# Optimization experiments

Measured on AMD Instinct MI355X. Metric: run time of the kernel, lower is better.

## Reference

```python
import jax, jax.numpy as jnp
import numpy as np

B, S, D = 524288, 10, 6  # batch of independent tiny attention problems; original module is one [10,6] sample


def setup_inputs() -> dict:
    key = jax.random.key(0)
    ks = jax.random.split(key, 7)
    bound = 1.0 / np.sqrt(D)  # torch nn.Linear default init range
    x = jax.random.normal(ks[0], (B, S, D), dtype=jnp.float32)
    Wk = jax.random.uniform(ks[1], (D, D), jnp.float32, -bound, bound)
    bk = jax.random.uniform(ks[2], (D,), jnp.float32, -bound, bound)
    Wq = jax.random.uniform(ks[3], (D, D), jnp.float32, -bound, bound)
    bq = jax.random.uniform(ks[4], (D,), jnp.float32, -bound, bound)
    Wv = jax.random.uniform(ks[5], (D, D), jnp.float32, -bound, bound)
    bv = jax.random.uniform(ks[6], (D,), jnp.float32, -bound, bound)
    return {"x": x, "Wk": Wk, "bk": bk, "Wq": Wq, "bq": bq, "Wv": Wv, "bv": bv}


def reference(x, Wk, bk, Wq, bq, Wv, bv):
    # Linear layers (torch stores W as [out,in]; y = x W^T + b)
    k = jnp.einsum('bsd,ed->bse', x, Wk) + bk  # [B,S,D]
    q = jnp.einsum('bsd,ed->bse', x, Wq) + bq
    v = jnp.einsum('bsd,ed->bse', x, Wv) + bv
    # per-query attention over the 10 keys (no scaling in original)
    scores = jax.nn.softmax(jnp.einsum('bqd,bkd->bqk', q, k), axis=-1)  # [B,S,S]
    out = jnp.einsum('bqk,bkd->bqd', scores, v)  # [B,S,D]
    # original sums attended vector over feature dim -> one scalar per query
    return jnp.sum(out, axis=-1)  # [B,S]
```

## Files before the change

kernel.cpp:

```cpp
#include <hip/hip_runtime.h>


#define NB 524288
#define S 10
#define D 6

__global__ void precompute_kernel(const float* __restrict__ Wk, const float* __restrict__ bk,
                                  const float* __restrict__ Wq, const float* __restrict__ bq,
                                  const float* __restrict__ Wv, const float* __restrict__ bv,
                                  float* __restrict__ ws) {
    int t = threadIdx.x;
    if (t < 36) {
        int d = t / 6, dp = t % 6;
        float g = 0.f;
        for (int e = 0; e < D; ++e) g += Wq[e * D + d] * Wk[e * D + dp];
        ws[t] = g;
    } else if (t < 42) {
        int dp = t - 36;
        float s = 0.f;
        for (int e = 0; e < D; ++e) s += bq[e] * Wk[e * D + dp];
        ws[t] = s;
    } else if (t < 48) {
        int d = t - 42;
        float s = 0.f;
        for (int e = 0; e < D; ++e) s += Wv[e * D + d];
        ws[t] = s;
    } else if (t == 48) {
        float s = 0.f;
        for (int e = 0; e < D; ++e) s += bv[e];
        ws[t] = s;
    }
}

__global__ __launch_bounds__(256) void attn_kernel(const float* __restrict__ x,
                                                   const float* __restrict__ ws,
                                                   float* __restrict__ out) {
    int b = blockIdx.x * blockDim.x + threadIdx.x;
    if (b >= NB) return;

    float G[36], w[6], wvs[6];
    #pragma unroll
    for (int i = 0; i < 36; ++i) G[i] = ws[i];
    #pragma unroll
    for (int i = 0; i < 6; ++i) w[i] = ws[36 + i];
    #pragma unroll
    for (int i = 0; i < 6; ++i) wvs[i] = ws[42 + i];
    float bvs = ws[48];

    const float4* xp = (const float4*)(x + (size_t)b * (S * D));
    float xv[S * D];
    #pragma unroll
    for (int i = 0; i < 15; ++i) {
        float4 v = xp[i];
        xv[4 * i + 0] = v.x;
        xv[4 * i + 1] = v.y;
        xv[4 * i + 2] = v.z;
        xv[4 * i + 3] = v.w;
    }

    float z[S * D], a[S], vs[S];
    #pragma unroll
    for (int k = 0; k < S; ++k) {
        #pragma unroll
        for (int d = 0; d < D; ++d) {
            float zz = 0.f;
            #pragma unroll
            for (int dp = 0; dp < D; ++dp) zz += G[d * 6 + dp] * xv[k * D + dp];
            z[k * D + d] = zz;
        }
        float ak = 0.f, vk = bvs;
        #pragma unroll
        for (int dp = 0; dp < D; ++dp) {
            ak += w[dp] * xv[k * D + dp];
            vk += wvs[dp] * xv[k * D + dp];
        }
        a[k] = ak;
        vs[k] = vk;
    }

    float o[S];
    #pragma unroll
    for (int q = 0; q < S; ++q) {
        float num = 0.f, den = 0.f;
        #pragma unroll
        for (int k = 0; k < S; ++k) {
            float s = a[k];
            #pragma unroll
            for (int d = 0; d < D; ++d) s += xv[q * D + d] * z[k * D + d];
            float e = __expf(s);
            den += e;
            num += e * vs[k];
        }
        o[q] = num * __builtin_amdgcn_rcpf(den);
    }

    float2* op = (float2*)(out + (size_t)b * S);
    #pragma unroll
    for (int i = 0; i < 5; ++i) op[i] = make_float2(o[2 * i + 0], o[2 * i + 1]);
}

extern "C" void kernel_launch(void* const* d_in, const int* in_sizes, int n_in,
                              void* d_out, int out_size, void* d_ws, size_t ws_size,
                              hipStream_t stream) {
    const float* x  = (const float*)d_in[0];
    const float* Wk = (const float*)d_in[1];
    const float* bk = (const float*)d_in[2];
    const float* Wq = (const float*)d_in[3];
    const float* bq = (const float*)d_in[4];
    const float* Wv = (const float*)d_in[5];
    const float* bv = (const float*)d_in[6];
    float* out = (float*)d_out;
    float* ws  = (float*)d_ws;

    precompute_kernel<<<1, 64, 0, stream>>>(Wk, bk, Wq, bq, Wv, bv, ws);
    attn_kernel<<<NB / 256, 256, 0, stream>>>(x, ws, out);
}
```

Measured before the change: 42.52 us.

## Stage inputs through padded LDS and split each batch item across two threads

Each block now loads 128 batch items with coalesced float4 reads into LDS rows padded to 61 floats, then assigns two threads per item, each handling five queries. Query-side projection (x_q·G) replaces the per-key z computation, so each thread holds far fewer registers. The goal is coalesced global loads, fewer VGPRs and higher occupancy (launch bounds request 5 waves), in exchange for redundant key-side work across the thread pair, LDS traffic and a block barrier. Output writes become stride-5 scalar stores.

```diff
diff --git a/kernel.cpp b/kernel.cpp
--- a/kernel.cpp
+++ b/kernel.cpp
@@ -4,6 +4,9 @@
 #define NB 524288
 #define S 10
 #define D 6
+#define TPB 256
+#define EPB 128
+#define ROW 61
 
 __global__ void precompute_kernel(const float* __restrict__ Wk, const float* __restrict__ bk,
                                   const float* __restrict__ Wq, const float* __restrict__ bq,
@@ -32,11 +35,12 @@
     }
 }
 
-__global__ __launch_bounds__(256) void attn_kernel(const float* __restrict__ x,
-                                                   const float* __restrict__ ws,
-                                                   float* __restrict__ out) {
-    int b = blockIdx.x * blockDim.x + threadIdx.x;
-    if (b >= NB) return;
+__global__ __launch_bounds__(TPB, 5) void attn_kernel(const float* __restrict__ x,
+                                                      const float* __restrict__ ws,
+                                                      float* __restrict__ out) {
+    __shared__ float xs[EPB * ROW];
+    const int t = threadIdx.x;
+    const int blk = blockIdx.x;
 
     float G[36], w[6], wvs[6];
     #pragma unroll
@@ -45,58 +49,65 @@
     for (int i = 0; i < 6; ++i) w[i] = ws[36 + i];
     #pragma unroll
     for (int i = 0; i < 6; ++i) wvs[i] = ws[42 + i];
-    float bvs = ws[48];
+    const float bvs = ws[48];
 
-    const float4* xp = (const float4*)(x + (size_t)b * (S * D));
-    float xv[S * D];
+    const float4* xg = (const float4*)x + (size_t)blk * (EPB * 15);
     #pragma unroll
-    for (int i = 0; i < 15; ++i) {
-        float4 v = xp[i];
-        xv[4 * i + 0] = v.x;
-        xv[4 * i + 1] = v.y;
-        xv[4 * i + 2] = v.z;
-        xv[4 * i + 3] = v.w;
+    for (int i = 0; i < 8; ++i) {
+        int f = t + TPB * i;
+        if (f < EPB * 15) {
+            float4 v = xg[f];
+            int e = f / 15, sub = f - e * 15;
+            float* dst = &xs[e * ROW + sub * 4];
+            dst[0] = v.x; dst[1] = v.y; dst[2] = v.z; dst[3] = v.w;
+        }
+    }
+    __syncthreads();
+
+    const int e = t >> 1;
+    const int h = t & 1;
+    const float* xe = &xs[e * ROW];
+
+    float tq[5][6];
+    #pragma unroll
+    for (int j = 0; j < 5; ++j) {
+        int q = h * 5 + j;
+        float xq[6];
+        #pragma unroll
+        for (int d = 0; d < 6; ++d) xq[d] = xe[q * 6 + d];
+        #pragma unroll
+        for (int dp = 0; dp < 6; ++dp) {
+            float s = 0.f;
+            #pragma unroll
+            for (int d = 0; d < 6; ++d) s += xq[d] * G[d * 6 + dp];
+            tq[j][dp] = s;
+        }
     }
 
-    float z[S * D], a[S], vs[S];
+    float num[5] = {0.f, 0.f, 0.f, 0.f, 0.f};
+    float den[5] = {0.f, 0.f, 0.f, 0.f, 0.f};
     #pragma unroll
     for (int k = 0; k < S; ++k) {
+        float xk[6];
         #pragma unroll
-        for (int d = 0; d < D; ++d) {
-            float zz = 0.f;
+        for (int d = 0; d < 6; ++d) xk[d] = xe[k * 6 + d];
+        float a = 0.f, vk = bvs;
+        #pragma unroll
+        for (int d = 0; d < 6; ++d) { a += w[d] * xk[d]; vk += wvs[d] * xk[d]; }
+        #pragma unroll
+        for (int j = 0; j < 5; ++j) {
+            float s = a;
             #pragma unroll
-            for (int dp = 0; dp < D; ++dp) zz += G[d * 6 + dp] * xv[k * D + dp];
-            z[k * D + d] = zz;
+            for (int d = 0; d < 6; ++d) s += tq[j][d] * xk[d];
+            float ex = __expf(s);
+            den[j] += ex;
+            num[j] += ex * vk;
         }
-        float ak = 0.f, vk = bvs;
-        #pragma unroll
-        for (int dp = 0; dp < D; ++dp) {
-            ak += w[dp] * xv[k * D + dp];
-            vk += wvs[dp] * xv[k * D + dp];
-        }
-        a[k] = ak;
-        vs[k] = vk;
     }
 
-    float o[S];
+    float* op = out + (size_t)blk * (EPB * S) + t * 5;
     #pragma unroll
-    for (int q = 0; q < S; ++q) {
-        float num = 0.f, den = 0.f;
-        #pragma unroll
-        for (int k = 0; k < S; ++k) {
-            float s = a[k];
-            #pragma unroll
-            for (int d = 0; d < D; ++d) s += xv[q * D + d] * z[k * D + d];
-            float e = __expf(s);
-            den += e;
-            num += e * vs[k];
-        }
-        o[q] = num * __builtin_amdgcn_rcpf(den);
-    }
-
-    float2* op = (float2*)(out + (size_t)b * S);
-    #pragma unroll
-    for (int i = 0; i < 5; ++i) op[i] = make_float2(o[2 * i + 0], o[2 * i + 1]);
+    for (int j = 0; j < 5; ++j) op[j] = num[j] * __builtin_amdgcn_rcpf(den[j]);
 }
 
 extern "C" void kernel_launch(void* const* d_in, const int* in_sizes, int n_in,
@@ -113,5 +124,5 @@
     float* ws  = (float*)d_ws;
 
     precompute_kernel<<<1, 64, 0, stream>>>(Wk, bk, Wq, bq, Wv, bv, ws);
-    attn_kernel<<<NB / 256, 256, 0, stream>>>(x, ws, out);
+    attn_kernel<<<NB / EPB, TPB, 0, stream>>>(x, ws, out);
 }
```

After: 127.7 us. 200% more time.

## Process four elements per thread with double-buffered register prefetch

Applied to the files above, without the earlier changes.

Each thread now handles four batch elements spaced a grid apart, loading the next element's 60 floats into a second register buffer while computing the current one. Weights are read through readfirstlane so they stay in scalar registers, and log2(e) is folded into the precomputed Gram matrix so exp2 replaces expf. The aim is to hide global load latency and cut per-thread setup, at the cost of higher register pressure (two 60-float buffers) and a quarter as many threads. The launch bound now requests two blocks per CU.

```diff
diff --git a/kernel.cpp b/kernel.cpp
--- a/kernel.cpp
+++ b/kernel.cpp
@@ -4,22 +4,29 @@
 #define NB 524288
 #define S 10
 #define D 6
+#define XFL 60
+#define TPB 256
+#define EPT 4
+#define NTHREADS (NB / EPT)
+#define NBLK (NTHREADS / TPB)
+#define ESTRIDE NTHREADS
 
 __global__ void precompute_kernel(const float* __restrict__ Wk, const float* __restrict__ bk,
                                   const float* __restrict__ Wq, const float* __restrict__ bq,
                                   const float* __restrict__ Wv, const float* __restrict__ bv,
                                   float* __restrict__ ws) {
+    const float LOG2E = 1.44269504088896340736f;
     int t = threadIdx.x;
     if (t < 36) {
         int d = t / 6, dp = t % 6;
         float g = 0.f;
         for (int e = 0; e < D; ++e) g += Wq[e * D + d] * Wk[e * D + dp];
-        ws[t] = g;
+        ws[t] = g * LOG2E;
     } else if (t < 42) {
         int dp = t - 36;
         float s = 0.f;
         for (int e = 0; e < D; ++e) s += bq[e] * Wk[e * D + dp];
-        ws[t] = s;
+        ws[t] = s * LOG2E;
     } else if (t < 48) {
         int d = t - 42;
         float s = 0.f;
@@ -32,71 +39,90 @@
     }
 }
 
-__global__ __launch_bounds__(256) void attn_kernel(const float* __restrict__ x,
-                                                   const float* __restrict__ ws,
-                                                   float* __restrict__ out) {
-    int b = blockIdx.x * blockDim.x + threadIdx.x;
-    if (b >= NB) return;
+__device__ __forceinline__ float sconst(const float* __restrict__ p, int i) {
+    return __int_as_float(__builtin_amdgcn_readfirstlane(__float_as_int(p[i])));
+}
+
+#define LOAD_ELEM(buf, eidx)                                                 \
+    {                                                                        \
+        const float4* _p = (const float4*)(x + (size_t)(eidx) * XFL);        \
+        _Pragma("unroll")                                                    \
+        for (int _i = 0; _i < 15; ++_i) {                                    \
+            float4 _v = _p[_i];                                              \
+            buf[4 * _i + 0] = _v.x;                                          \
+            buf[4 * _i + 1] = _v.y;                                          \
+            buf[4 * _i + 2] = _v.z;                                          \
+            buf[4 * _i + 3] = _v.w;                                          \
+        }                                                                    \
+    }
+
+#define COMPUTE_ELEM(xv, eidx)                                               \
+    {                                                                        \
+        float z[XFL], a[S], vs[S];                                           \
+        _Pragma("unroll")                                                    \
+        for (int _k = 0; _k < S; ++_k) {                                     \
+            float _ak = 0.f, _vk = bvs;                                      \
+            _Pragma("unroll")                                                \
+            for (int _d = 0; _d < D; ++_d) {                                 \
+                float _xk = xv[_k * D + _d];                                 \
+                _ak += w[_d] * _xk;                                          \
+                _vk += wvs[_d] * _xk;                                        \
+            }                                                                \
+            a[_k] = _ak; vs[_k] = _vk;                                       \
+            _Pragma("unroll")                                                \
+            for (int _d = 0; _d < D; ++_d) {                                 \
+                float _zz = 0.f;                                             \
+                _Pragma("unroll")                                            \
+                for (int _dp = 0; _dp < D; ++_dp)                            \
+                    _zz += G[_d * D + _dp] * xv[_k * D + _dp];               \
+                z[_k * D + _d] = _zz;                                        \
+            }                                                                \
+        }                                                                    \
+        float o[S];                                                          \
+        _Pragma("unroll")                                                    \
+        for (int _q = 0; _q < S; ++_q) {                                     \
+            float _num = 0.f, _den = 0.f;                                    \
+            _Pragma("unroll")                                                \
+            for (int _k = 0; _k < S; ++_k) {                                 \
+                float _s = a[_k];                                            \
+                _Pragma("unroll")                                            \
+                for (int _d = 0; _d < D; ++_d)                               \
+                    _s += xv[_q * D + _d] * z[_k * D + _d];                  \
+                float _ex = __builtin_amdgcn_exp2f(_s);                      \
+                _den += _ex; _num += _ex * vs[_k];                           \
+            }                                                                \
+            o[_q] = _num * __builtin_amdgcn_rcpf(_den);                      \
+        }                                                                    \
+        float2* _op = (float2*)(out + (size_t)(eidx) * S);                   \
+        _Pragma("unroll")                                                    \
+        for (int _i = 0; _i < 5; ++_i)                                       \
+            _op[_i] = make_float2(o[2 * _i], o[2 * _i + 1]);                 \
+    }
+
+__global__ __launch_bounds__(TPB, 2) void attn_kernel(const float* __restrict__ x,
+                                                      const float* __restrict__ ws,
+                                                      float* __restrict__ out) {
+    const int g = blockIdx.x * TPB + threadIdx.x;
 
     float G[36], w[6], wvs[6];
     #pragma unroll
-    for (int i = 0; i < 36; ++i) G[i] = ws[i];
+    for (int i = 0; i < 36; ++i) G[i] = sconst(ws, i);
     #pragma unroll
-    for (int i = 0; i < 6; ++i) w[i] = ws[36 + i];
+    for (int i = 0; i < 6; ++i) w[i] = sconst(ws, 36 + i);
     #pragma unroll
-    for (int i = 0; i < 6; ++i) wvs[i] = ws[42 + i];
-    float bvs = ws[48];
+    for (int i = 0; i < 6; ++i) wvs[i] = sconst(ws, 42 + i);
+    const float bvs = sconst(ws, 48);
 
-    const float4* xp = (const float4*)(x + (size_t)b * (S * D));
-    float xv[S * D];
-    #pragma unroll
-    for (int i = 0; i < 15; ++i) {
-        float4 v = xp[i];
-        xv[4 * i + 0] = v.x;
-        xv[4 * i + 1] = v.y;
-        xv[4 * i + 2] = v.z;
-        xv[4 * i + 3] = v.w;
-    }
+    float bufA[XFL], bufB[XFL];
 
-    float z[S * D], a[S], vs[S];
-    #pragma unroll
-    for (int k = 0; k < S; ++k) {
-        #pragma unroll
-        for (int d = 0; d < D; ++d) {
-            float zz = 0.f;
-            #pragma unroll
-            for (int dp = 0; dp < D; ++dp) zz += G[d * 6 + dp] * xv[k * D + dp];
-            z[k * D + d] = zz;
-        }
-        float ak = 0.f, vk = bvs;
-        #pragma unroll
-        for (int dp = 0; dp < D; ++dp) {
-            ak += w[dp] * xv[k * D + dp];
-            vk += wvs[dp] * xv[k * D + dp];
-        }
-        a[k] = ak;
-        vs[k] = vk;
-    }
-
-    float o[S];
-    #pragma unroll
-    for (int q = 0; q < S; ++q) {
-        float num = 0.f, den = 0.f;
-        #pragma unroll
-        for (int k = 0; k < S; ++k) {
-            float s = a[k];
-            #pragma unroll
-            for (int d = 0; d < D; ++d) s += xv[q * D + d] * z[k * D + d];
-            float e = __expf(s);
-            den += e;
-            num += e * vs[k];
-        }
-        o[q] = num * __builtin_amdgcn_rcpf(den);
-    }
-
-    float2* op = (float2*)(out + (size_t)b * S);
-    #pragma unroll
-    for (int i = 0; i < 5; ++i) op[i] = make_float2(o[2 * i + 0], o[2 * i + 1]);
+    LOAD_ELEM(bufA, g + 0 * ESTRIDE);
+    LOAD_ELEM(bufB, g + 1 * ESTRIDE);
+    COMPUTE_ELEM(bufA, g + 0 * ESTRIDE);
+    LOAD_ELEM(bufA, g + 2 * ESTRIDE);
+    COMPUTE_ELEM(bufB, g + 1 * ESTRIDE);
+    LOAD_ELEM(bufB, g + 3 * ESTRIDE);
+    COMPUTE_ELEM(bufA, g + 2 * ESTRIDE);
+    COMPUTE_ELEM(bufB, g + 3 * ESTRIDE);
 }
 
 extern "C" void kernel_launch(void* const* d_in, const int* in_sizes, int n_in,
@@ -113,5 +139,5 @@
     float* ws  = (float*)d_ws;
 
     precompute_kernel<<<1, 64, 0, stream>>>(Wk, bk, Wq, bq, Wv, bv, ws);
-    attn_kernel<<<NB / 256, 256, 0, stream>>>(x, ws, out);
+    attn_kernel<<<NBLK, TPB, 0, stream>>>(x, ws, out);
 }
```

After: 51.01 us. 1.2x slower.
